# Kernel optimization log

Hardware: AMD Instinct MI355X
Metric: run time of the kernel (lower is better)

The kernel has to match this reference:

```python
import jax, jax.numpy as jnp
import numpy as np

B, T, D = 2, 2048, 1024
H, DK, DV = 16, 64, 64
DFF = 4096
EPS = 1e-6


def layer_norm(x, gamma, beta):
    # Matches the torch module: unbiased std (ddof=1), eps added to std,
    # gamma multiplied before dividing by (std + eps).
    mean = x.mean(axis=-1, keepdims=True)
    std = x.std(axis=-1, ddof=1, keepdims=True)
    return (x - mean) * gamma / (std + EPS) + beta


def setup_inputs() -> dict:
    key = jax.random.key(0)
    ks = jax.random.split(key, 8)
    s = 0.02
    return {
        "x": jax.random.normal(ks[0], (B, T, D), dtype=jnp.float32),
        "w_q": jax.random.normal(ks[1], (D, H * DK), dtype=jnp.float32) * s,
        "w_k": jax.random.normal(ks[2], (D, H * DK), dtype=jnp.float32) * s,
        "w_v": jax.random.normal(ks[3], (D, H * DV), dtype=jnp.float32) * s,
        "w_o": jax.random.normal(ks[4], (H * DV, D), dtype=jnp.float32) * s,
        "b_o": jnp.zeros((D,), dtype=jnp.float32),
        "w_fc1": jax.random.normal(ks[5], (D, DFF), dtype=jnp.float32) * s,
        "b_fc1": jnp.zeros((DFF,), dtype=jnp.float32),
        "w_fc2": jax.random.normal(ks[6], (DFF, D), dtype=jnp.float32) * s,
        "b_fc2": jnp.zeros((D,), dtype=jnp.float32),
        "ln1_g": jnp.ones((D,), dtype=jnp.float32),
        "ln1_b": jnp.zeros((D,), dtype=jnp.float32),
        "ln2_g": jnp.ones((D,), dtype=jnp.float32),
        "ln2_b": jnp.zeros((D,), dtype=jnp.float32),
    }


def attention(h, w_q, w_k, w_v, w_o, b_o):
    b, t, _ = h.shape
    q = (h @ w_q).reshape(b, t, H, DK).transpose(0, 2, 1, 3)  # [b,h,t,dk]
    k = (h @ w_k).reshape(b, t, H, DK).transpose(0, 2, 1, 3)
    v = (h @ w_v).reshape(b, t, H, DV).transpose(0, 2, 1, 3)
    scores = jnp.einsum('bhqk,bhmk->bhqm', q, k)              # [b,h,t,t]
    causal = jnp.triu(jnp.ones((t, t), dtype=bool), k=1)
    scores = jnp.where(causal, -jnp.inf, scores)
    attn = jax.nn.softmax(scores / jnp.sqrt(jnp.float32(DK)), axis=-1)
    ctx = jnp.einsum('bhqm,bhmv->bhqv', attn, v)              # [b,h,t,dv]
    ctx = ctx.transpose(0, 2, 1, 3).reshape(b, t, H * DV)
    return ctx @ w_o + b_o


def reference(x, w_q, w_k, w_v, w_o, b_o, w_fc1, b_fc1, w_fc2, b_fc2,
              ln1_g, ln1_b, ln2_g, ln2_b):
    x = x + attention(layer_norm(x, ln1_g, ln1_b), w_q, w_k, w_v, w_o, b_o)
    h = layer_norm(x, ln2_g, ln2_b)
    mlp = jax.nn.gelu(h @ w_fc1 + b_fc1, approximate=False) @ w_fc2 + b_fc2
    return x + mlp
```

## Files before the change

kernel.cpp:

```cpp
#include <hip/hip_runtime.h>
#include <hip/hip_bf16.h>
#include <cstdint>

#define Bz 2
#define Tz 2048
#define Dz 1024
#define Hz 16
#define NR (Bz*Tz)

typedef __bf16 bf16;
typedef __bf16 bf16x8 __attribute__((ext_vector_type(8)));
typedef __bf16 bf16x4 __attribute__((ext_vector_type(4)));
typedef short  s16x4  __attribute__((ext_vector_type(4)));
typedef float  f32x4  __attribute__((ext_vector_type(4)));

typedef unsigned int u32as1 __attribute__((address_space(1)));
typedef unsigned int u32as3 __attribute__((address_space(3)));

__device__ __forceinline__ void gl2lds16(const void* gp, void* lp) {
    __builtin_amdgcn_global_load_lds((u32as1*)gp, (u32as3*)lp, 16, 0, 0);
}

__global__ void k_transpose_cvt(const float* __restrict__ W, bf16* __restrict__ WT,
                                int K, int N, float scale) {
    __shared__ float tile[32][33];
    const int n0 = blockIdx.x * 32, k0 = blockIdx.y * 32;
    const int tx = threadIdx.x, ty = threadIdx.y;
#pragma unroll
    for (int i = 0; i < 4; i++)
        tile[ty + i*8][tx] = W[(size_t)(k0 + ty + i*8) * N + n0 + tx];
    __syncthreads();
#pragma unroll
    for (int i = 0; i < 4; i++)
        WT[(size_t)(n0 + ty + i*8) * K + k0 + tx] = (bf16)(tile[tx][ty + i*8] * scale);
}

__global__ void k_vtrans(const bf16* __restrict__ qkv, bf16* __restrict__ Vt) {
    __shared__ bf16 tile[64][72];
    const int t0 = blockIdx.x * 64;
    const int bh = blockIdx.y;
    const int b = bh >> 4, h = bh & 15;
    const int tid = threadIdx.x;
    const int tr = tid >> 3, c8 = (tid & 7) * 8;
    const bf16* src = qkv + (size_t)b * Tz * 3072 + 2048 + h * 64;
#pragma unroll
    for (int i = 0; i < 2; i++) {
        bf16x8 v = *(const bf16x8*)(src + (size_t)(t0 + i*32 + tr) * 3072 + c8);
        *(bf16x8*)&tile[i*32 + tr][c8] = v;
    }
    __syncthreads();
    bf16* dst = Vt + (size_t)bh * 64 * Tz + t0;
#pragma unroll
    for (int i = 0; i < 2; i++) {
        const int vr = i*32 + tr;
        bf16x8 o;
#pragma unroll
        for (int j = 0; j < 8; j++) o[j] = tile[c8 + j][vr];
        *(bf16x8*)(dst + (size_t)vr * Tz + c8) = o;
    }
}

__global__ void k_layernorm(const float* __restrict__ X, const float* __restrict__ gam,
                            const float* __restrict__ bet, bf16* __restrict__ out) {
    const int row = blockIdx.x, t = threadIdx.x;
    const float4 v = ((const float4*)(X + (size_t)row * Dz))[t];
    float s  = v.x + v.y + v.z + v.w;
    float ss = v.x*v.x + v.y*v.y + v.z*v.z + v.w*v.w;
#pragma unroll
    for (int o = 1; o < 64; o <<= 1) { s += __shfl_xor(s, o); ss += __shfl_xor(ss, o); }
    __shared__ float rs[4], rss[4];
    if ((t & 63) == 0) { rs[t >> 6] = s; rss[t >> 6] = ss; }
    __syncthreads();
    s  = rs[0] + rs[1] + rs[2] + rs[3];
    ss = rss[0] + rss[1] + rss[2] + rss[3];
    const float mean = s * (1.f / Dz);
    const float var  = fmaxf((ss - s * mean) * (1.f / (Dz - 1)), 0.f);
    const float inv  = 1.f / (sqrtf(var) + 1e-6f);
    const float4 gv = ((const float4*)gam)[t];
    const float4 bv = ((const float4*)bet)[t];
    bf16x4 o;
    o[0] = (bf16)((v.x - mean) * gv.x * inv + bv.x);
    o[1] = (bf16)((v.y - mean) * gv.y * inv + bv.y);
    o[2] = (bf16)((v.z - mean) * gv.z * inv + bv.z);
    o[3] = (bf16)((v.w - mean) * gv.w * inv + bv.w);
    *(bf16x4*)(out + (size_t)row * Dz + t * 4) = o;
}

__global__ __launch_bounds__(256) void k_gemm(
    const bf16* __restrict__ A, const bf16* __restrict__ BT,
    int M, int N, int K,
    const float* __restrict__ bias, const float* __restrict__ resid,
    float* __restrict__ Cf, bf16* __restrict__ Cb, int act)
{
    __shared__ bf16 lA[128 * 64];
    __shared__ bf16 lB[128 * 64];
    const int tid = threadIdx.x;
    const int w = tid >> 6, lane = tid & 63;
    const int q = lane >> 4, l16 = lane & 15;
    const int m0 = blockIdx.y * 128, n0 = blockIdx.x * 128;
    const int wm = (w >> 1) * 64, wn = (w & 1) * 64;

    const int srow = lane >> 3;
    const int skg  = (lane & 7) ^ srow;
    const bf16* Ab = A  + (size_t)(m0 + w * 32 + srow) * K + skg * 8;
    const bf16* Bb = BT + (size_t)(n0 + w * 32 + srow) * K + skg * 8;
    bf16* lAw = lA + w * 2048;
    bf16* lBw = lB + w * 2048;

    f32x4 acc[4][4] = {};

    for (int k0 = 0; k0 < K; k0 += 64) {
#pragma unroll
        for (int i = 0; i < 4; i++) {
            gl2lds16(Ab + (size_t)i * 8 * K + k0, lAw + i * 512);
            gl2lds16(Bb + (size_t)i * 8 * K + k0, lBw + i * 512);
        }
        __syncthreads();
#pragma unroll
        for (int kh = 0; kh < 2; kh++) {
            const int sl = (((kh * 4 + q) ^ (l16 & 7)) * 8);
            bf16x8 af[4], bfr[4];
#pragma unroll
            for (int t = 0; t < 4; t++) {
                af[t]  = *(const bf16x8*)(lA + (wm + t * 16 + l16) * 64 + sl);
                bfr[t] = *(const bf16x8*)(lB + (wn + t * 16 + l16) * 64 + sl);
            }
#pragma unroll
            for (int i = 0; i < 4; i++)
#pragma unroll
                for (int j = 0; j < 4; j++)
                    acc[i][j] = __builtin_amdgcn_mfma_f32_16x16x32_bf16(
                        af[i], bfr[j], acc[i][j], 0, 0, 0);
        }
        __syncthreads();
    }

#pragma unroll
    for (int i = 0; i < 4; i++) {
        const int gr = m0 + wm + i * 16 + q * 4;
#pragma unroll
        for (int j = 0; j < 4; j++) {
            const int gc = n0 + wn + j * 16 + l16;
            const float bv = bias ? bias[gc] : 0.f;
#pragma unroll
            for (int r = 0; r < 4; r++) {
                float v = acc[i][j][r] + bv;
                if (act) v = 0.5f * v * (1.f + erff(v * 0.70710678118f));
                const size_t idx = (size_t)(gr + r) * N + gc;
                if (resid) v += resid[idx];
                if (Cf) Cf[idx] = v;
                else    Cb[idx] = (bf16)v;
            }
        }
    }
}

__global__ __launch_bounds__(256) void k_attn(const bf16* __restrict__ qkv,
                                              const bf16* __restrict__ Vt,
                                              bf16* __restrict__ ctx)
{
    __shared__ __align__(16) char smem[34816];
    bf16* lK = (bf16*)smem;
    bf16* lV = (bf16*)(smem + 16384);
    f32x4* sAcc = (f32x4*)smem;
    float*  sM  = (float*)(smem + 32768);
    float*  sL  = (float*)(smem + 33792);

    const int tid = threadIdx.x, lane = tid & 63, w = tid >> 6;
    const int l16 = lane & 15, quad = lane >> 4;
    const int wq = w & 1, ws = w >> 1;
    const int qb = gridDim.x - 1 - blockIdx.x;
    const int h = blockIdx.y, b = blockIdx.z;
    const int q0 = qb * 64 + wq * 32;

    const bf16* Qp  = qkv + (size_t)b * Tz * 3072 + h * 64;
    const bf16* Kp  = Qp + 1024;
    const bf16* Vtp = Vt + (size_t)(b * Hz + h) * 64 * Tz;

    const int krow  = tid >> 3;
    const int kslot = (tid & 7) ^ (krow & 7);
    const bf16* Kg = Kp + (size_t)krow * 3072 + kslot * 8;
    const int vrow  = tid >> 4;
    const int vslot = (tid & 15) ^ (vrow & 7);
    const bf16* Vg = Vtp + (size_t)vrow * Tz + vslot * 8;

    bf16x8 qf[2][2];
#pragma unroll
    for (int g = 0; g < 2; g++)
#pragma unroll
        for (int kh = 0; kh < 2; kh++)
            qf[g][kh] = *(const bf16x8*)(Qp + (size_t)(q0 + g*16 + l16) * 3072 + kh*32 + quad*8);

    f32x4 acc[2][4] = {};
    float m[2] = {-1e30f, -1e30f}, l[2] = {0.f, 0.f};

    const int keyEnd = qb * 64 + 64;
    for (int ktB = 0; ktB < keyEnd; ktB += 128) {
        if (ktB) __syncthreads();
#pragma unroll
        for (int s = 0; s < 4; s++) {
            gl2lds16(Kg + (size_t)(ktB + s * 32) * 3072, lK + s * 2048 + w * 512);
            gl2lds16(Vg + (size_t)s * 16 * Tz + ktB,     lV + s * 2048 + w * 512);
        }
        __syncthreads();

        const int kt = ktB + ws * 64;
        if (kt <= q0 + 31) {
            f32x4 sv[2][4];
            const int sw = l16 & 7;
#pragma unroll
            for (int c = 0; c < 4; c++) {
                const int R = ws * 64 + c * 16 + l16;
                bf16x8 kf0 = *(const bf16x8*)(lK + R * 64 + ((quad     ^ sw) * 8));
                bf16x8 kf1 = *(const bf16x8*)(lK + R * 64 + (((4+quad) ^ sw) * 8));
#pragma unroll
                for (int g = 0; g < 2; g++) {
                    f32x4 z = {0.f, 0.f, 0.f, 0.f};
                    z = __builtin_amdgcn_mfma_f32_16x16x32_bf16(kf0, qf[g][0], z, 0, 0, 0);
                    z = __builtin_amdgcn_mfma_f32_16x16x32_bf16(kf1, qf[g][1], z, 0, 0, 0);
                    sv[g][c] = z;
                }
            }
            if (kt + 63 > q0) {
#pragma unroll
                for (int g = 0; g < 2; g++)
#pragma unroll
                    for (int c = 0; c < 4; c++)
#pragma unroll
                        for (int r = 0; r < 4; r++)
                            if (kt + c*16 + quad*4 + r > q0 + g*16 + l16) sv[g][c][r] = -1e30f;
            }
            float tm[2];
#pragma unroll
            for (int g = 0; g < 2; g++) {
                float t0 = fmaxf(fmaxf(sv[g][0][0], sv[g][0][1]), fmaxf(sv[g][0][2], sv[g][0][3]));
                float t1 = fmaxf(fmaxf(sv[g][1][0], sv[g][1][1]), fmaxf(sv[g][1][2], sv[g][1][3]));
                float t2 = fmaxf(fmaxf(sv[g][2][0], sv[g][2][1]), fmaxf(sv[g][2][2], sv[g][2][3]));
                float t3 = fmaxf(fmaxf(sv[g][3][0], sv[g][3][1]), fmaxf(sv[g][3][2], sv[g][3][3]));
                float t4 = fmaxf(fmaxf(t0, t1), fmaxf(t2, t3));
                t4 = fmaxf(t4, __shfl_xor(t4, 16));
                t4 = fmaxf(t4, __shfl_xor(t4, 32));
                tm[g] = t4;
            }
            if (__any((tm[0] > m[0]) || (tm[1] > m[1]))) {
#pragma unroll
                for (int g = 0; g < 2; g++) {
                    const float mn = fmaxf(m[g], tm[g]);
                    const float a  = __expf(m[g] - mn);
                    m[g] = mn;
                    l[g] *= a;
#pragma unroll
                    for (int vt = 0; vt < 4; vt++)
#pragma unroll
                        for (int r = 0; r < 4; r++) acc[g][vt][r] *= a;
                }
            }
            float ts0 = 0.f, ts1 = 0.f;
#pragma unroll
            for (int c = 0; c < 4; c++) {
                s16x4 vf[4];
                const int gslot = ws * 8 + c * 2 + (quad >> 1);
#pragma unroll
                for (int vt = 0; vt < 4; vt++) {
                    const int Rv = vt * 16 + l16;
                    vf[vt] = *(const s16x4*)(lV + Rv * 128 + ((gslot ^ (Rv & 7)) * 8)
                                             + (quad & 1) * 4);
                }
#pragma unroll
                for (int g = 0; g < 2; g++) {
                    bf16x4 t;
#pragma unroll
                    for (int r = 0; r < 4; r++) {
                        const float p = __expf(sv[g][c][r] - m[g]);
                        if (g == 0) ts0 += p; else ts1 += p;
                        t[r] = (bf16)p;
                    }
                    const s16x4 pb = __builtin_bit_cast(s16x4, t);
#pragma unroll
                    for (int vt = 0; vt < 4; vt++)
                        acc[g][vt] = __builtin_amdgcn_mfma_f32_16x16x16bf16_1k(
                            vf[vt], pb, acc[g][vt], 0, 0, 0);
                }
            }
            ts0 += __shfl_xor(ts0, 16); ts0 += __shfl_xor(ts0, 32);
            ts1 += __shfl_xor(ts1, 16); ts1 += __shfl_xor(ts1, 32);
            l[0] += ts0; l[1] += ts1;
        }
    }

    __syncthreads();
    if (ws == 1) {
#pragma unroll
        for (int g = 0; g < 2; g++) {
            sM[(wq*2 + g) * 64 + lane] = m[g];
            sL[(wq*2 + g) * 64 + lane] = l[g];
#pragma unroll
            for (int vt = 0; vt < 4; vt++)
                sAcc[((wq*2 + g) * 4 + vt) * 64 + lane] = acc[g][vt];
        }
    }
    __syncthreads();
    if (ws == 0) {
#pragma unroll
        for (int g = 0; g < 2; g++) {
            const float m1 = sM[(wq*2 + g) * 64 + lane], l1 = sL[(wq*2 + g) * 64 + lane];
            const float M  = fmaxf(m[g], m1);
            const float a0 = __expf(m[g] - M), a1 = __expf(m1 - M);
            const float inv = 1.f / (l[g] * a0 + l1 * a1);
#pragma unroll
            for (int vt = 0; vt < 4; vt++) {
                const f32x4 o1 = sAcc[((wq*2 + g) * 4 + vt) * 64 + lane];
                bf16x4 o;
#pragma unroll
                for (int r = 0; r < 4; r++)
                    o[r] = (bf16)((acc[g][vt][r] * a0 + o1[r] * a1) * inv);
                *(bf16x4*)(ctx + (size_t)(b * Tz + q0 + g*16 + l16) * 1024
                           + h * 64 + vt * 16 + quad * 4) = o;
            }
        }
    }
}

extern "C" void kernel_launch(void* const* d_in, const int* in_sizes, int n_in,
                              void* d_out, int out_size, void* d_ws, size_t ws_size,
                              hipStream_t stream)
{
    const float* x     = (const float*)d_in[0];
    const float* w_q   = (const float*)d_in[1];
    const float* w_k   = (const float*)d_in[2];
    const float* w_v   = (const float*)d_in[3];
    const float* w_o   = (const float*)d_in[4];
    const float* b_o   = (const float*)d_in[5];
    const float* w_fc1 = (const float*)d_in[6];
    const float* b_fc1 = (const float*)d_in[7];
    const float* w_fc2 = (const float*)d_in[8];
    const float* b_fc2 = (const float*)d_in[9];
    const float* ln1_g = (const float*)d_in[10];
    const float* ln1_b = (const float*)d_in[11];
    const float* ln2_g = (const float*)d_in[12];
    const float* ln2_b = (const float*)d_in[13];
    float* out = (float*)d_out;

    char* p = (char*)d_ws;
    bf16* wqkvT = (bf16*)p; p += (size_t)3072 * 1024 * 2;
    bf16* woT   = (bf16*)p; p += (size_t)1024 * 1024 * 2;
    bf16* wfc1T = (bf16*)p; p += (size_t)4096 * 1024 * 2;
    bf16* wfc2T = (bf16*)p; p += (size_t)1024 * 4096 * 2;
    bf16* h1    = (bf16*)p; p += (size_t)NR * 1024 * 2;
    bf16* qkv   = (bf16*)p; p += (size_t)NR * 3072 * 2;
    bf16* ctx   = (bf16*)p; p += (size_t)NR * 1024 * 2;
    float* y    = (float*)p; p += (size_t)NR * 1024 * 4;
    bf16* h2    = (bf16*)p; p += (size_t)NR * 1024 * 2;
    bf16* g     = (bf16*)p; p += (size_t)NR * 4096 * 2;
    bf16* Vt    = h1;

    const dim3 tb(32, 8);
    k_transpose_cvt<<<dim3(32, 32),  tb, 0, stream>>>(w_q,   wqkvT,             1024, 1024, 0.125f);
    k_transpose_cvt<<<dim3(32, 32),  tb, 0, stream>>>(w_k,   wqkvT + 1024*1024, 1024, 1024, 1.f);
    k_transpose_cvt<<<dim3(32, 32),  tb, 0, stream>>>(w_v,   wqkvT + 2048*1024, 1024, 1024, 1.f);
    k_transpose_cvt<<<dim3(32, 32),  tb, 0, stream>>>(w_o,   woT,               1024, 1024, 1.f);
    k_transpose_cvt<<<dim3(128, 32), tb, 0, stream>>>(w_fc1, wfc1T,             1024, 4096, 1.f);
    k_transpose_cvt<<<dim3(32, 128), tb, 0, stream>>>(w_fc2, wfc2T,             4096, 1024, 1.f);

    k_layernorm<<<NR, 256, 0, stream>>>(x, ln1_g, ln1_b, h1);
    k_gemm<<<dim3(3072/128, NR/128), 256, 0, stream>>>(h1, wqkvT, NR, 3072, 1024,
                                                       nullptr, nullptr, nullptr, qkv, 0);
    k_vtrans<<<dim3(Tz/64, Bz*Hz), 256, 0, stream>>>(qkv, Vt);
    k_attn<<<dim3(Tz/64, Hz, Bz), 256, 0, stream>>>(qkv, Vt, ctx);
    k_gemm<<<dim3(1024/128, NR/128), 256, 0, stream>>>(ctx, woT, NR, 1024, 1024,
                                                       b_o, x, y, nullptr, 0);
    k_layernorm<<<NR, 256, 0, stream>>>(y, ln2_g, ln2_b, h2);
    k_gemm<<<dim3(4096/128, NR/128), 256, 0, stream>>>(h2, wfc1T, NR, 4096, 1024,
                                                       b_fc1, nullptr, nullptr, g, 1);
    k_gemm<<<dim3(1024/128, NR/128), 256, 0, stream>>>(g, wfc2T, NR, 1024, 4096,
                                                       b_fc2, y, out, nullptr, 0);
    (void)in_sizes; (void)n_in; (void)out_size; (void)ws_size;
}
```

Measured before the change: 472.8 us.

## Add split-K with separate reduction kernel for N=1024 GEMMs

The output-projection and FC2 GEMMs (N=1024) launch only 256 blocks, roughly one per compute unit. This splits K across two blocks per tile, doubling the block count to improve latency hiding. Each split writes fp32 partial tiles to workspace, and a new elementwise reduce kernel sums them and then applies the bias, optional GELU and residual. The cost is extra fp32 partial traffic and an added kernel launch per GEMM. The partials reuse buffers that are dead at that point, and the FC2 partials spill past h1 into the dead qkv and ctx region.

```diff
diff --git a/kernel.cpp b/kernel.cpp
--- a/kernel.cpp
+++ b/kernel.cpp
@@ -90,7 +90,8 @@
     const bf16* __restrict__ A, const bf16* __restrict__ BT,
     int M, int N, int K,
     const float* __restrict__ bias, const float* __restrict__ resid,
-    float* __restrict__ Cf, bf16* __restrict__ Cb, int act)
+    float* __restrict__ Cf, bf16* __restrict__ Cb, int act,
+    float* __restrict__ Cpart, int nsplit)
 {
     __shared__ bf16 lA[128 * 64];
     __shared__ bf16 lB[128 * 64];
@@ -109,7 +110,9 @@
 
     f32x4 acc[4][4] = {};
 
-    for (int k0 = 0; k0 < K; k0 += 64) {
+    const int kPer = K / nsplit;
+    const int kBeg = blockIdx.z * kPer, kEnd = kBeg + kPer;
+    for (int k0 = kBeg; k0 < kEnd; k0 += 64) {
 #pragma unroll
         for (int i = 0; i < 4; i++) {
             gl2lds16(Ab + (size_t)i * 8 * K + k0, lAw + i * 512);
@@ -133,6 +136,22 @@
                         af[i], bfr[j], acc[i][j], 0, 0, 0);
         }
         __syncthreads();
+    }
+
+    if (nsplit > 1) {
+        float* P = Cpart + (size_t)blockIdx.z * M * N;
+#pragma unroll
+        for (int i = 0; i < 4; i++) {
+            const int gr = m0 + wm + i * 16 + q * 4;
+#pragma unroll
+            for (int j = 0; j < 4; j++) {
+                const int gc = n0 + wn + j * 16 + l16;
+#pragma unroll
+                for (int r = 0; r < 4; r++)
+                    P[(size_t)(gr + r) * N + gc] = acc[i][j][r];
+            }
+        }
+        return;
     }
 
 #pragma unroll
@@ -152,6 +171,39 @@
                 else    Cb[idx] = (bf16)v;
             }
         }
+    }
+}
+
+__global__ __launch_bounds__(256) void k_reduce(
+    const float* __restrict__ part, int nsplit, size_t MN, int N,
+    const float* __restrict__ bias, const float* __restrict__ resid,
+    float* __restrict__ Cf, bf16* __restrict__ Cb, int act)
+{
+    const size_t i4 = ((size_t)blockIdx.x * 256 + threadIdx.x) * 4;
+    float4 v = *(const float4*)(part + i4);
+    for (int s = 1; s < nsplit; s++) {
+        const float4 p = *(const float4*)(part + s * MN + i4);
+        v.x += p.x; v.y += p.y; v.z += p.z; v.w += p.w;
+    }
+    const int col = (int)(i4 % N);
+    if (bias) {
+        const float4 bv = *(const float4*)(bias + col);
+        v.x += bv.x; v.y += bv.y; v.z += bv.z; v.w += bv.w;
+    }
+    if (act) {
+        v.x = 0.5f * v.x * (1.f + erff(v.x * 0.70710678118f));
+        v.y = 0.5f * v.y * (1.f + erff(v.y * 0.70710678118f));
+        v.z = 0.5f * v.z * (1.f + erff(v.z * 0.70710678118f));
+        v.w = 0.5f * v.w * (1.f + erff(v.w * 0.70710678118f));
+    }
+    if (resid) {
+        const float4 rv = *(const float4*)(resid + i4);
+        v.x += rv.x; v.y += rv.y; v.z += rv.z; v.w += rv.w;
+    }
+    if (Cf) *(float4*)(Cf + i4) = v;
+    else {
+        bf16x4 o; o[0] = (bf16)v.x; o[1] = (bf16)v.y; o[2] = (bf16)v.z; o[3] = (bf16)v.w;
+        *(bf16x4*)(Cb + i4) = o;
     }
 }
 
@@ -353,6 +405,8 @@
     bf16* h2    = (bf16*)p; p += (size_t)NR * 1024 * 2;
     bf16* g     = (bf16*)p; p += (size_t)NR * 4096 * 2;
     bf16* Vt    = h1;
+    float* projPart = (float*)g;
+    float* fc2Part  = (float*)h1;
 
     const dim3 tb(32, 8);
     k_transpose_cvt<<<dim3(32, 32),  tb, 0, stream>>>(w_q,   wqkvT,             1024, 1024, 0.125f);
@@ -364,15 +418,25 @@
 
     k_layernorm<<<NR, 256, 0, stream>>>(x, ln1_g, ln1_b, h1);
     k_gemm<<<dim3(3072/128, NR/128), 256, 0, stream>>>(h1, wqkvT, NR, 3072, 1024,
-                                                       nullptr, nullptr, nullptr, qkv, 0);
+                                                       nullptr, nullptr, nullptr, qkv, 0,
+                                                       nullptr, 1);
     k_vtrans<<<dim3(Tz/64, Bz*Hz), 256, 0, stream>>>(qkv, Vt);
     k_attn<<<dim3(Tz/64, Hz, Bz), 256, 0, stream>>>(qkv, Vt, ctx);
-    k_gemm<<<dim3(1024/128, NR/128), 256, 0, stream>>>(ctx, woT, NR, 1024, 1024,
-                                                       b_o, x, y, nullptr, 0);
+
+    k_gemm<<<dim3(1024/128, NR/128, 2), 256, 0, stream>>>(ctx, woT, NR, 1024, 1024,
+                                                          nullptr, nullptr, nullptr, nullptr, 0,
+                                                          projPart, 2);
+    k_reduce<<<(size_t)NR * 1024 / 1024, 256, 0, stream>>>(projPart, 2, (size_t)NR * 1024, 1024,
+                                                           b_o, x, y, nullptr, 0);
+
     k_layernorm<<<NR, 256, 0, stream>>>(y, ln2_g, ln2_b, h2);
     k_gemm<<<dim3(4096/128, NR/128), 256, 0, stream>>>(h2, wfc1T, NR, 4096, 1024,
-                                                       b_fc1, nullptr, nullptr, g, 1);
-    k_gemm<<<dim3(1024/128, NR/128), 256, 0, stream>>>(g, wfc2T, NR, 1024, 4096,
-                                                       b_fc2, y, out, nullptr, 0);
+                                                       b_fc1, nullptr, nullptr, g, 1,
+                                                       nullptr, 1);
+    k_gemm<<<dim3(1024/128, NR/128, 2), 256, 0, stream>>>(g, wfc2T, NR, 1024, 4096,
+                                                          nullptr, nullptr, nullptr, nullptr, 0,
+                                                          fc2Part, 2);
+    k_reduce<<<(size_t)NR * 1024 / 1024, 256, 0, stream>>>(fc2Part, 2, (size_t)NR * 1024, 1024,
+                                                           b_fc2, y, out, nullptr, 0);
     (void)in_sizes; (void)n_in; (void)out_size; (void)ws_size;
 }
```

After: 428.9 us. 9.3% less time.
